# Kernel optimization log

Hardware: AMD Instinct MI355X
Metric: run time of the kernel (lower is better)

The kernel has to match this reference:

```python
import jax, jax.numpy as jnp
import numpy as np

B, N, H, F = 4, 512, 4096, 11008   # batch, seq, hidden, intermediate
L, R, RANK = 1, 16, 16             # layers stored, num adapters, lora rank
SCALE = 0.5                        # lora_scale


def setup_inputs() -> dict:
    key = jax.random.key(0)
    ks = jax.random.split(key, 12)
    nrm = lambda k, shape, fan: (jax.random.normal(k, shape, jnp.float32) * (fan ** -0.5))
    inp = {
        "x": jax.random.normal(ks[0], (B, N, H), jnp.float32),
        "W_gate": nrm(ks[1], (F, H), H),
        "W_up": nrm(ks[2], (F, H), H),
        "W_down": nrm(ks[3], (H, F), F),
        # LoRA tables: [num_layers, num_adapters, rank, in] and [num_layers, num_adapters, out, rank]
        "A_gate": nrm(ks[4], (L, R, RANK, H), H),
        "B_gate": nrm(ks[5], (L, R, F, RANK), RANK),
        "A_up": nrm(ks[6], (L, R, RANK, H), H),
        "B_up": nrm(ks[7], (L, R, F, RANK), RANK),
        "A_down": nrm(ks[8], (L, R, RANK, F), F),
        "B_down": nrm(ks[9], (L, R, H, RANK), RANK),
        "lora_indices": jax.random.randint(ks[10], (B,), 0, R),
        "layer_idx": 0,
    }
    return inp


def reference(x, W_gate, W_up, W_down, A_gate, B_gate, A_up, B_up,
              A_down, B_down, lora_indices, layer_idx):
    def lora_add(base, inp, A, B):
        # gather per-sequence adapter slices, then rank-r batched matmuls
        Ab = A[layer_idx][lora_indices]  # [B, r, in]
        Bb = B[layer_idx][lora_indices]  # [B, out, r]
        t = jnp.einsum('bri,bni->bnr', Ab, inp)        # down-project to rank
        return base + jnp.einsum('bor,bnr->bno', Bb, t) * SCALE

    gate = lora_add(jnp.einsum('bnh,fh->bnf', x, W_gate), x, A_gate, B_gate)
    up = lora_add(jnp.einsum('bnh,fh->bnf', x, W_up), x, A_up, B_up)
    act = jax.nn.silu(gate) * up                        # SwiGLU
    down = lora_add(jnp.einsum('bnf,hf->bnh', act, W_down), act, A_down, B_down)
    return down
```

## Files before the change

kernel.cpp:

```cpp
#include <hip/hip_runtime.h>
#include <hip/hip_bf16.h>

typedef __bf16 bf16x8 __attribute__((ext_vector_type(8)));
typedef float  f32x4  __attribute__((ext_vector_type(4)));
typedef unsigned short u16;

#define GLDS16(gsrc, ldst)                                                        \
  __builtin_amdgcn_global_load_lds(                                               \
      (const __attribute__((address_space(1))) unsigned int*)(gsrc),              \
      (__attribute__((address_space(3))) unsigned int*)(ldst), 16, 0, 0)

#define BAR() __builtin_amdgcn_s_barrier()
#define WAIT_LGKM0() asm volatile("s_waitcnt lgkmcnt(0)" ::: "memory")
#define WAIT_VM4() asm volatile("s_waitcnt vmcnt(4)" ::: "memory")

__device__ __forceinline__ u16 f2b(float f) {
  unsigned int u = __builtin_bit_cast(unsigned int, f);
  u = (u + 0x7fffu + ((u >> 16) & 1u)) >> 16;
  return (u16)u;
}
__device__ __forceinline__ float b2f(u16 b) {
  unsigned int u = ((unsigned int)b) << 16;
  return __builtin_bit_cast(float, u);
}

__global__ __launch_bounds__(256) void cvt_kernel(const float4* __restrict__ in,
                                                  ushort4* __restrict__ out, int n4) {
  int i = blockIdx.x * blockDim.x + threadIdx.x;
  int stride = gridDim.x * blockDim.x;
  for (; i < n4; i += stride) {
    float4 v = in[i];
    ushort4 o;
    o.x = f2b(v.x); o.y = f2b(v.y); o.z = f2b(v.z); o.w = f2b(v.w);
    out[i] = o;
  }
}

__global__ __launch_bounds__(256) void lora_t2(const u16* __restrict__ Xb, int K,
                                               const float* __restrict__ A1,
                                               const float* __restrict__ A2,
                                               const int* __restrict__ lidx,
                                               const int* __restrict__ layer,
                                               u16* __restrict__ t1,
                                               u16* __restrict__ t2) {
  __shared__ float red1[4][64][4];
  __shared__ float red2[4][64][4];
  const int lane = threadIdx.x & 63, wid = threadIdx.x >> 6;
  const int m0 = blockIdx.x * 16;
  const int li = lidx[m0 >> 9];
  const size_t abase = ((size_t)layer[0] * 16 + li) * 16 * (size_t)K;
  const int r = lane & 15, kg = lane >> 4;
  const int Kq = K >> 2, kb = wid * Kq;
  f32x4 acc1 = {0.f, 0.f, 0.f, 0.f}, acc2 = {0.f, 0.f, 0.f, 0.f};
  for (int k0 = kb; k0 < kb + Kq; k0 += 32) {
    bf16x8 a = *(const bf16x8*)&Xb[(size_t)(m0 + r) * K + k0 + kg * 8];
    const float* ap = A1 + abase + (size_t)r * K + k0 + kg * 8;
    float4 f0 = *(const float4*)ap;
    float4 f1 = *(const float4*)(ap + 4);
    bf16x8 b;
    b[0] = (__bf16)f0.x; b[1] = (__bf16)f0.y; b[2] = (__bf16)f0.z; b[3] = (__bf16)f0.w;
    b[4] = (__bf16)f1.x; b[5] = (__bf16)f1.y; b[6] = (__bf16)f1.z; b[7] = (__bf16)f1.w;
    acc1 = __builtin_amdgcn_mfma_f32_16x16x32_bf16(a, b, acc1, 0, 0, 0);
    if (A2) {
      const float* ap2 = A2 + abase + (size_t)r * K + k0 + kg * 8;
      float4 g0 = *(const float4*)ap2;
      float4 g1 = *(const float4*)(ap2 + 4);
      bf16x8 b2;
      b2[0] = (__bf16)g0.x; b2[1] = (__bf16)g0.y; b2[2] = (__bf16)g0.z; b2[3] = (__bf16)g0.w;
      b2[4] = (__bf16)g1.x; b2[5] = (__bf16)g1.y; b2[6] = (__bf16)g1.z; b2[7] = (__bf16)g1.w;
      acc2 = __builtin_amdgcn_mfma_f32_16x16x32_bf16(a, b2, acc2, 0, 0, 0);
    }
  }
#pragma unroll
  for (int j = 0; j < 4; ++j) {
    red1[wid][lane][j] = acc1[j];
    if (A2) red2[wid][lane][j] = acc2[j];
  }
  __syncthreads();
  if (wid == 0) {
#pragma unroll
    for (int j = 0; j < 4; ++j) {
      int m = m0 + kg * 4 + j;
      float v1 = red1[0][lane][j] + red1[1][lane][j] + red1[2][lane][j] + red1[3][lane][j];
      t1[(size_t)m * 16 + r] = f2b(0.5f * v1);
      if (A2) {
        float v2 = red2[0][lane][j] + red2[1][lane][j] + red2[2][lane][j] + red2[3][lane][j];
        t2[(size_t)m * 16 + r] = f2b(0.5f * v2);
      }
    }
  }
}

#define RD_A(dst, buf, mh) do {                                                \
    _Pragma("unroll")                                                          \
    for (int mf_ = 0; mf_ < 4; ++mf_)                                          \
      _Pragma("unroll")                                                        \
      for (int ks_ = 0; ks_ < 2; ++ks_) {                                      \
        int row_ = wm * 128 + (mh) * 64 + mf_ * 16 + lr;                       \
        int sl_ = (ks_ * 4 + kg) ^ rx;                                         \
        dst[mf_][ks_] = *(const bf16x8*)&sA[(buf) * 16384 + row_ * 64 + sl_ * 8]; \
      }                                                                        \
  } while (0)

#define RD_B(dst, buf, nh) do {                                                \
    _Pragma("unroll")                                                          \
    for (int nf_ = 0; nf_ < 2; ++nf_)                                          \
      _Pragma("unroll")                                                        \
      for (int ks_ = 0; ks_ < 2; ++ks_) {                                      \
        int row_ = wn * 64 + (nh) * 32 + nf_ * 16 + lr;                        \
        int sl_ = (ks_ * 4 + kg) ^ rx;                                         \
        dst[nf_][ks_] = *(const bf16x8*)&sB[(buf) * 16384 + row_ * 64 + sl_ * 8]; \
      }                                                                        \
  } while (0)

#define MMA_Q(AF, BF, mb, nb) do {                                             \
    __builtin_amdgcn_s_setprio(1);                                             \
    _Pragma("unroll")                                                          \
    for (int mf_ = 0; mf_ < 4; ++mf_)                                          \
      _Pragma("unroll")                                                        \
      for (int nf_ = 0; nf_ < 2; ++nf_)                                        \
        _Pragma("unroll")                                                      \
        for (int ks_ = 0; ks_ < 2; ++ks_)                                      \
          acc[(mb) + mf_][(nb) + nf_] = __builtin_amdgcn_mfma_f32_16x16x32_bf16( \
              AF[mf_][ks_], BF[nf_][ks_], acc[(mb) + mf_][(nb) + nf_], 0, 0, 0); \
    __builtin_amdgcn_s_setprio(0);                                             \
  } while (0)

#define STAGE(buf, half, kt) do {                                              \
    int r0_ = ((half) & 1) * 128;                                              \
    const u16* gs_ = ((half) < 2)                                              \
        ? (Xb + (size_t)(m0 + r0_) * 4096 + (size_t)(kt) * 64)                 \
        : (W + (size_t)(n0 + r0_) * 4096 + (size_t)(kt) * 64);                 \
    u16* ld_ = (((half) < 2) ? sA : sB) + (buf) * 16384 + r0_ * 64;            \
    _Pragma("unroll")                                                          \
    for (int i_ = 0; i_ < 2; ++i_) {                                           \
      int ub_ = (wid << 6) + i_ * 512;                                         \
      int un_ = ub_ + lane;                                                    \
      int ur_ = un_ >> 3, us_ = (un_ & 7) ^ (ur_ & 7);                         \
      GLDS16(gs_ + (size_t)ur_ * 4096 + us_ * 8, ld_ + ub_ * 8);               \
    }                                                                          \
  } while (0)

__global__ __launch_bounds__(512, 2) void gemm_gup8(
    const u16* __restrict__ Xb, const u16* __restrict__ Wg, const u16* __restrict__ Wu,
    const u16* __restrict__ tg, const u16* __restrict__ tu,
    const float* __restrict__ Bg, const float* __restrict__ Bu,
    const int* __restrict__ lidx, const int* __restrict__ layer,
    u16* __restrict__ gout, u16* __restrict__ uout) {
  constexpr int F = 11008;
  const int b = blockIdx.x;
  const int xcd = b & 7, j = b >> 3;
  const int ny = xcd + 8 * (j >> 3);
  const int mx = j & 7;
  if (ny >= 86) return;
  extern __shared__ u16 smem[];
  u16* sA = smem;
  u16* sB = smem + 32768;
  const int tid = threadIdx.x, lane = tid & 63, wid = tid >> 6;
  const int lr = lane & 15, kg = lane >> 4, rx = lr & 7;
  const int wm = wid >> 2, wn = wid & 3;
  const bool isUp = ny >= 43;
  const int m0 = mx * 256;
  const int n0 = (isUp ? ny - 43 : ny) * 256;
  const u16* W = isUp ? Wu : Wg;
  const u16* tb = isUp ? tu : tg;
  const float* Bw = isUp ? Bu : Bg;
  u16* ob = isUp ? uout : gout;

  f32x4 acc[8][4] = {};
  bf16x8 a0[4][2], a1[4][2], b0[2][2], b1[2][2];

  STAGE(0, 0, 0); STAGE(0, 1, 0); STAGE(0, 2, 0); STAGE(0, 3, 0);
  STAGE(1, 2, 1); STAGE(1, 3, 1);
  WAIT_VM4(); BAR();

#pragma unroll 1
  for (int u = 0; u < 32; ++u) {
    const int ktA = (2 * u + 1) & 63;
    const int kt0 = (2 * u + 2) & 63;
    const int kt1 = (2 * u + 3) & 63;
    RD_A(a0, 0, 0); RD_B(b0, 0, 0);
    STAGE(1, 0, ktA);
    BAR(); WAIT_LGKM0();
    MMA_Q(a0, b0, 0, 0);
    BAR();
    RD_B(b1, 0, 1);
    STAGE(1, 1, ktA);
    BAR(); WAIT_LGKM0();
    MMA_Q(a0, b1, 0, 2);
    BAR();
    RD_A(a1, 0, 1);
    STAGE(0, 2, kt0);
    BAR(); WAIT_LGKM0();
    MMA_Q(a1, b1, 4, 2);
    BAR();
    STAGE(0, 3, kt0);
    BAR();
    MMA_Q(a1, b0, 4, 0);
    WAIT_VM4();
    BAR();
    RD_A(a0, 1, 0); RD_B(b0, 1, 0);
    STAGE(0, 0, kt0);
    BAR(); WAIT_LGKM0();
    MMA_Q(a0, b0, 0, 0);
    BAR();
    RD_B(b1, 1, 1);
    STAGE(0, 1, kt0);
    BAR(); WAIT_LGKM0();
    MMA_Q(a0, b1, 0, 2);
    BAR();
    RD_A(a1, 1, 1);
    STAGE(1, 2, kt1);
    BAR(); WAIT_LGKM0();
    MMA_Q(a1, b1, 4, 2);
    BAR();
    STAGE(1, 3, kt1);
    BAR();
    MMA_Q(a1, b0, 4, 0);
    WAIT_VM4();
    BAR();
  }

  const int li = lidx[m0 >> 9];
  const size_t bbase = ((size_t)layer[0] * 16 + li) * (size_t)F * 16;
  bf16x8 la[8], lb[4];
  const bf16x8 zz = {};
#pragma unroll
  for (int mf = 0; mf < 8; ++mf) {
    int row = m0 + wm * 128 + mf * 16 + lr;
    la[mf] = (kg < 2) ? *(const bf16x8*)&tb[(size_t)row * 16 + kg * 8] : zz;
  }
#pragma unroll
  for (int nf = 0; nf < 4; ++nf) {
    int col = n0 + wn * 64 + nf * 16 + lr;
    if (kg < 2) {
      const float* bp = Bw + bbase + (size_t)col * 16 + kg * 8;
      float4 f0 = *(const float4*)bp;
      float4 f1 = *(const float4*)(bp + 4);
      bf16x8 v;
      v[0] = (__bf16)f0.x; v[1] = (__bf16)f0.y; v[2] = (__bf16)f0.z; v[3] = (__bf16)f0.w;
      v[4] = (__bf16)f1.x; v[5] = (__bf16)f1.y; v[6] = (__bf16)f1.z; v[7] = (__bf16)f1.w;
      lb[nf] = v;
    } else lb[nf] = zz;
  }
#pragma unroll
  for (int mf = 0; mf < 8; ++mf)
#pragma unroll
    for (int nf = 0; nf < 4; ++nf)
      acc[mf][nf] = __builtin_amdgcn_mfma_f32_16x16x32_bf16(la[mf], lb[nf], acc[mf][nf], 0, 0, 0);

#pragma unroll
  for (int mf = 0; mf < 8; ++mf)
#pragma unroll
    for (int nf = 0; nf < 4; ++nf)
#pragma unroll
      for (int j2 = 0; j2 < 4; ++j2) {
        int row = m0 + wm * 128 + mf * 16 + kg * 4 + j2;
        int col = n0 + wn * 64 + nf * 16 + lr;
        ob[(size_t)row * F + col] = f2b(acc[mf][nf][j2]);
      }
}

#define STAGE_D(buf, half, kt) do {                                           \
    int r0_ = ((half) & 1) * 128;                                             \
    const u16* gs_ = ((half) < 2)                                             \
        ? (Ab + (size_t)(m0 + r0_) * 11008 + (size_t)(kt) * 64)               \
        : (Wd + (size_t)(n0 + r0_) * 11008 + (size_t)(kt) * 64);              \
    u16* ld_ = (((half) < 2) ? sA : sB) + (buf) * 16384 + r0_ * 64;           \
    _Pragma("unroll")                                                         \
    for (int i_ = 0; i_ < 2; ++i_) {                                          \
      int ub_ = (wid << 6) + i_ * 512;                                        \
      int un_ = ub_ + lane;                                                   \
      int ur_ = un_ >> 3, us_ = (un_ & 7) ^ (ur_ & 7);                        \
      GLDS16(gs_ + (size_t)ur_ * 11008 + us_ * 8, ld_ + ub_ * 8);             \
    }                                                                         \
  } while (0)

#define KT(t) (kbase + ((t) >= 86 ? (t) - 86 : (t)))

__global__ __launch_bounds__(512, 2) void gemm_down8(
    const u16* __restrict__ Ab, const u16* __restrict__ Wd,
    const u16* __restrict__ td, const float* __restrict__ Bd,
    const int* __restrict__ lidx, const int* __restrict__ layer,
    float* __restrict__ P0, float* __restrict__ P1) {
  constexpr int H = 4096;
  extern __shared__ u16 smem[];
  u16* sA = smem;
  u16* sB = smem + 32768;
  const int tid = threadIdx.x, lane = tid & 63, wid = tid >> 6;
  const int lr = lane & 15, kg = lane >> 4, rx = lr & 7;
  const int wm = wid >> 2, wn = wid & 3;
  const int m0 = blockIdx.x * 256, n0 = blockIdx.y * 256;
  const int kbase = blockIdx.z * 86;
  float* P = blockIdx.z ? P1 : P0;

  f32x4 acc[8][4] = {};
  bf16x8 a0[4][2], a1[4][2], b0[2][2], b1[2][2];

  STAGE_D(0, 0, KT(0)); STAGE_D(0, 1, KT(0)); STAGE_D(0, 2, KT(0)); STAGE_D(0, 3, KT(0));
  STAGE_D(1, 2, KT(1)); STAGE_D(1, 3, KT(1));
  WAIT_VM4(); BAR();

#pragma unroll 1
  for (int u = 0; u < 43; ++u) {
    const int ktA = KT(2 * u + 1);
    const int kt0 = KT(2 * u + 2);
    const int kt1 = KT(2 * u + 3);
    RD_A(a0, 0, 0); RD_B(b0, 0, 0);
    STAGE_D(1, 0, ktA);
    BAR(); WAIT_LGKM0();
    MMA_Q(a0, b0, 0, 0);
    BAR();
    RD_B(b1, 0, 1);
    STAGE_D(1, 1, ktA);
    BAR(); WAIT_LGKM0();
    MMA_Q(a0, b1, 0, 2);
    BAR();
    RD_A(a1, 0, 1);
    STAGE_D(0, 2, kt0);
    BAR(); WAIT_LGKM0();
    MMA_Q(a1, b1, 4, 2);
    BAR();
    STAGE_D(0, 3, kt0);
    BAR();
    MMA_Q(a1, b0, 4, 0);
    WAIT_VM4();
    BAR();
    RD_A(a0, 1, 0); RD_B(b0, 1, 0);
    STAGE_D(0, 0, kt0);
    BAR(); WAIT_LGKM0();
    MMA_Q(a0, b0, 0, 0);
    BAR();
    RD_B(b1, 1, 1);
    STAGE_D(0, 1, kt0);
    BAR(); WAIT_LGKM0();
    MMA_Q(a0, b1, 0, 2);
    BAR();
    RD_A(a1, 1, 1);
    STAGE_D(1, 2, kt1);
    BAR(); WAIT_LGKM0();
    MMA_Q(a1, b1, 4, 2);
    BAR();
    STAGE_D(1, 3, kt1);
    BAR();
    MMA_Q(a1, b0, 4, 0);
    WAIT_VM4();
    BAR();
  }

  if (blockIdx.z == 0) {
    const int li = lidx[m0 >> 9];
    const size_t bbase = ((size_t)layer[0] * 16 + li) * (size_t)H * 16;
    bf16x8 la[8], lb[4];
    const bf16x8 zz = {};
#pragma unroll
    for (int mf = 0; mf < 8; ++mf) {
      int row = m0 + wm * 128 + mf * 16 + lr;
      la[mf] = (kg < 2) ? *(const bf16x8*)&td[(size_t)row * 16 + kg * 8] : zz;
    }
#pragma unroll
    for (int nf = 0; nf < 4; ++nf) {
      int col = n0 + wn * 64 + nf * 16 + lr;
      if (kg < 2) {
        const float* bp = Bd + bbase + (size_t)col * 16 + kg * 8;
        float4 f0 = *(const float4*)bp;
        float4 f1 = *(const float4*)(bp + 4);
        bf16x8 v;
        v[0] = (__bf16)f0.x; v[1] = (__bf16)f0.y; v[2] = (__bf16)f0.z; v[3] = (__bf16)f0.w;
        v[4] = (__bf16)f1.x; v[5] = (__bf16)f1.y; v[6] = (__bf16)f1.z; v[7] = (__bf16)f1.w;
        lb[nf] = v;
      } else lb[nf] = zz;
    }
#pragma unroll
    for (int mf = 0; mf < 8; ++mf)
#pragma unroll
      for (int nf = 0; nf < 4; ++nf)
        acc[mf][nf] = __builtin_amdgcn_mfma_f32_16x16x32_bf16(la[mf], lb[nf], acc[mf][nf], 0, 0, 0);
  }

#pragma unroll
  for (int mf = 0; mf < 8; ++mf)
#pragma unroll
    for (int nf = 0; nf < 4; ++nf)
#pragma unroll
      for (int j = 0; j < 4; ++j) {
        int row = m0 + wm * 128 + mf * 16 + kg * 4 + j;
        int col = n0 + wn * 64 + nf * 16 + lr;
        P[(size_t)row * H + col] = acc[mf][nf][j];
      }
}

__global__ __launch_bounds__(256) void combine_down(
    const float4* __restrict__ P0, const float4* __restrict__ P1,
    float4* __restrict__ out) {
  int gid = blockIdx.x * 256 + threadIdx.x;
  float4 p0 = P0[gid], p1 = P1[gid];
  out[gid] = make_float4(p0.x + p1.x, p0.y + p1.y, p0.z + p1.z, p0.w + p1.w);
}

__global__ __launch_bounds__(256) void swiglu_kernel(uint4* __restrict__ g,
                                                     const uint4* __restrict__ u, int n) {
  int i = blockIdx.x * 256 + threadIdx.x, st = gridDim.x * 256;
  for (; i < n; i += st) {
    uint4 gv = g[i], uv = u[i], ov;
    unsigned* gw = (unsigned*)&gv;
    unsigned* uw = (unsigned*)&uv;
    unsigned* ow = (unsigned*)&ov;
#pragma unroll
    for (int q = 0; q < 4; ++q) {
      float g0 = __builtin_bit_cast(float, gw[q] << 16);
      float g1 = __builtin_bit_cast(float, gw[q] & 0xffff0000u);
      float u0 = __builtin_bit_cast(float, uw[q] << 16);
      float u1 = __builtin_bit_cast(float, uw[q] & 0xffff0000u);
      float a0 = g0 / (1.f + __expf(-g0)) * u0;
      float a1 = g1 / (1.f + __expf(-g1)) * u1;
      ow[q] = (unsigned)f2b(a0) | ((unsigned)f2b(a1) << 16);
    }
    g[i] = ov;
  }
}

extern "C" void kernel_launch(void* const* d_in, const int* in_sizes, int n_in,
                              void* d_out, int out_size, void* d_ws, size_t ws_size,
                              hipStream_t stream) {
  const float* x  = (const float*)d_in[0];
  const float* Wg = (const float*)d_in[1];
  const float* Wu = (const float*)d_in[2];
  const float* Wd = (const float*)d_in[3];
  const float* Ag = (const float*)d_in[4];
  const float* Bg = (const float*)d_in[5];
  const float* Au = (const float*)d_in[6];
  const float* Bu = (const float*)d_in[7];
  const float* Ad = (const float*)d_in[8];
  const float* Bd = (const float*)d_in[9];
  const int* lidx = (const int*)d_in[10];
  const int* lay  = (const int*)d_in[11];
  float* out = (float*)d_out;

  char* ws = (char*)d_ws;
  u16*  xb   = (u16*)(ws + 0);
  u16*  wgb  = (u16*)(ws + 16777216);
  u16*  wub  = (u16*)(ws + 106954752);
  u16*  gbuf = (u16*)(ws + 197132288);
  u16*  ubuf = (u16*)(ws + 242221056);
  u16*  tg   = (u16*)(ws + 287309824);
  u16*  tu   = (u16*)(ws + 287375360);
  u16*  td   = (u16*)(ws + 287440896);
  u16*  wdb2 = wgb;
  float* P0  = (float*)ubuf;
  float* P1  = (float*)wub;

  hipFuncSetAttribute(reinterpret_cast<const void*>(gemm_gup8),
                      hipFuncAttributeMaxDynamicSharedMemorySize, 131072);
  hipFuncSetAttribute(reinterpret_cast<const void*>(gemm_down8),
                      hipFuncAttributeMaxDynamicSharedMemorySize, 131072);

  cvt_kernel<<<1024, 256, 0, stream>>>((const float4*)x,  (ushort4*)xb,  8388608 / 4);
  cvt_kernel<<<2048, 256, 0, stream>>>((const float4*)Wg, (ushort4*)wgb, 45088768 / 4);
  cvt_kernel<<<2048, 256, 0, stream>>>((const float4*)Wu, (ushort4*)wub, 45088768 / 4);

  lora_t2<<<128, 256, 0, stream>>>(xb, 4096, Ag, Au, lidx, lay, tg, tu);

  gemm_gup8<<<dim3(704), 512, 131072, stream>>>(xb, wgb, wub, tg, tu, Bg, Bu,
                                                lidx, lay, gbuf, ubuf);

  swiglu_kernel<<<2048, 256, 0, stream>>>((uint4*)gbuf, (const uint4*)ubuf, 2818048);

  cvt_kernel<<<2048, 256, 0, stream>>>((const float4*)Wd, (ushort4*)wdb2, 45088768 / 4);

  lora_t2<<<128, 256, 0, stream>>>(gbuf, 11008, Ad, nullptr, lidx, lay, td, nullptr);

  gemm_down8<<<dim3(8, 16, 2), 512, 131072, stream>>>(gbuf, wdb2, td, Bd, lidx, lay, P0, P1);

  combine_down<<<8192, 256, 0, stream>>>((const float4*)P0, (const float4*)P1, (float4*)out);
}
```

Before: 774.7 us.

## Overlap W_down conversion with gate/up GEMM and use atomic split-K reduction

Extra blocks are appended to the gate/up GEMM launch to convert W_down to bf16 into a separate workspace region, so the conversion overlaps with the GEMM instead of running as its own kernel. This only happens when the workspace is large enough; otherwise the separate conversion kernel still runs. The split-K down GEMM now atomically adds into a zeroed output, which removes the partial buffers and the combine kernel. In exchange it adds a memset and float atomics, and the summation order becomes nondeterministic. The extra blocks also run at the heavy GEMM's launch bounds and shared-memory size, which may compete with GEMM blocks for occupancy.

```diff
diff --git a/kernel.cpp b/kernel.cpp
--- a/kernel.cpp
+++ b/kernel.cpp
@@ -146,9 +146,20 @@
     const u16* __restrict__ tg, const u16* __restrict__ tu,
     const float* __restrict__ Bg, const float* __restrict__ Bu,
     const int* __restrict__ lidx, const int* __restrict__ layer,
-    u16* __restrict__ gout, u16* __restrict__ uout) {
+    u16* __restrict__ gout, u16* __restrict__ uout,
+    const float4* __restrict__ Wdf, ushort4* __restrict__ wdb3) {
   constexpr int F = 11008;
   const int b = blockIdx.x;
+  if (b >= 704) {
+    int i = (b - 704) * 512 + threadIdx.x;
+    for (; i < 11272192; i += 256 * 512) {
+      float4 v = Wdf[i];
+      ushort4 o;
+      o.x = f2b(v.x); o.y = f2b(v.y); o.z = f2b(v.z); o.w = f2b(v.w);
+      wdb3[i] = o;
+    }
+    return;
+  }
   const int xcd = b & 7, j = b >> 3;
   const int ny = xcd + 8 * (j >> 3);
   const int mx = j & 7;
@@ -282,7 +293,7 @@
     const u16* __restrict__ Ab, const u16* __restrict__ Wd,
     const u16* __restrict__ td, const float* __restrict__ Bd,
     const int* __restrict__ lidx, const int* __restrict__ layer,
-    float* __restrict__ P0, float* __restrict__ P1) {
+    float* __restrict__ out) {
   constexpr int H = 4096;
   extern __shared__ u16 smem[];
   u16* sA = smem;
@@ -292,7 +303,6 @@
   const int wm = wid >> 2, wn = wid & 3;
   const int m0 = blockIdx.x * 256, n0 = blockIdx.y * 256;
   const int kbase = blockIdx.z * 86;
-  float* P = blockIdx.z ? P1 : P0;
 
   f32x4 acc[8][4] = {};
   bf16x8 a0[4][2], a1[4][2], b0[2][2], b1[2][2];
@@ -386,16 +396,8 @@
       for (int j = 0; j < 4; ++j) {
         int row = m0 + wm * 128 + mf * 16 + kg * 4 + j;
         int col = n0 + wn * 64 + nf * 16 + lr;
-        P[(size_t)row * H + col] = acc[mf][nf][j];
+        unsafeAtomicAdd(&out[(size_t)row * H + col], acc[mf][nf][j]);
       }
-}
-
-__global__ __launch_bounds__(256) void combine_down(
-    const float4* __restrict__ P0, const float4* __restrict__ P1,
-    float4* __restrict__ out) {
-  int gid = blockIdx.x * 256 + threadIdx.x;
-  float4 p0 = P0[gid], p1 = P1[gid];
-  out[gid] = make_float4(p0.x + p1.x, p0.y + p1.y, p0.z + p1.z, p0.w + p1.w);
 }
 
 __global__ __launch_bounds__(256) void swiglu_kernel(uint4* __restrict__ g,
@@ -446,31 +448,33 @@
   u16*  tg   = (u16*)(ws + 287309824);
   u16*  tu   = (u16*)(ws + 287375360);
   u16*  td   = (u16*)(ws + 287440896);
-  u16*  wdb2 = wgb;
-  float* P0  = (float*)ubuf;
-  float* P1  = (float*)wub;
+  u16*  wdb3 = (u16*)(ws + 287506432);
+  const bool bigws = ws_size >= 377683968ull;
+  u16*  wdb  = bigws ? wdb3 : wgb;
 
   hipFuncSetAttribute(reinterpret_cast<const void*>(gemm_gup8),
                       hipFuncAttributeMaxDynamicSharedMemorySize, 131072);
   hipFuncSetAttribute(reinterpret_cast<const void*>(gemm_down8),
                       hipFuncAttributeMaxDynamicSharedMemorySize, 131072);
 
+  hipMemsetAsync(out, 0, 33554432, stream);
+
   cvt_kernel<<<1024, 256, 0, stream>>>((const float4*)x,  (ushort4*)xb,  8388608 / 4);
   cvt_kernel<<<2048, 256, 0, stream>>>((const float4*)Wg, (ushort4*)wgb, 45088768 / 4);
   cvt_kernel<<<2048, 256, 0, stream>>>((const float4*)Wu, (ushort4*)wub, 45088768 / 4);
 
   lora_t2<<<128, 256, 0, stream>>>(xb, 4096, Ag, Au, lidx, lay, tg, tu);
 
-  gemm_gup8<<<dim3(704), 512, 131072, stream>>>(xb, wgb, wub, tg, tu, Bg, Bu,
-                                                lidx, lay, gbuf, ubuf);
+  gemm_gup8<<<dim3(bigws ? 960 : 704), 512, 131072, stream>>>(
+      xb, wgb, wub, tg, tu, Bg, Bu, lidx, lay, gbuf, ubuf,
+      (const float4*)Wd, (ushort4*)wdb3);
 
   swiglu_kernel<<<2048, 256, 0, stream>>>((uint4*)gbuf, (const uint4*)ubuf, 2818048);
 
-  cvt_kernel<<<2048, 256, 0, stream>>>((const float4*)Wd, (ushort4*)wdb2, 45088768 / 4);
+  if (!bigws)
+    cvt_kernel<<<2048, 256, 0, stream>>>((const float4*)Wd, (ushort4*)wdb, 45088768 / 4);
 
   lora_t2<<<128, 256, 0, stream>>>(gbuf, 11008, Ad, nullptr, lidx, lay, td, nullptr);
 
-  gemm_down8<<<dim3(8, 16, 2), 512, 131072, stream>>>(gbuf, wdb2, td, Bd, lidx, lay, P0, P1);
-
-  combine_down<<<8192, 256, 0, stream>>>((const float4*)P0, (const float4*)P1, (float4*)out);
-}
+  gemm_down8<<<dim3(8, 16, 2), 512, 131072, stream>>>(gbuf, wdb, td, Bd, lidx, lay, out);
+}
```

Result: slower. 790.4 us (+2.0%).
